# Optimization experiments

Hardware: AMD Instinct MI355X
Metric: run time of the kernel (lower is better)

## Reference

```python
import jax, jax.numpy as jnp
import numpy as np

E, H, BLOCK = 1024, 64, 2048

def setup_inputs() -> dict:
    key = jax.random.key(0)
    kx, kk, kq, kv = jax.random.split(key, 4)
    s = 1.0 / np.sqrt(E)
    return {
        "x": jax.random.normal(kx, (16, 2048, E), dtype=jnp.float32),
        "Wk": jax.random.uniform(kk, (E, H), jnp.float32, -s, s),
        "Wq": jax.random.uniform(kq, (E, H), jnp.float32, -s, s),
        "Wv": jax.random.uniform(kv, (E, H), jnp.float32, -s, s),
    }

def reference(x, Wk, Wq, Wv):
    B, T, C = x.shape
    k = x @ Wk  # [B,T,H]
    q = x @ Wq
    v = x @ Wv
    scale = jnp.asarray(H, x.dtype) ** -0.5
    wei = jnp.einsum("bth,bsh->bts", q, k) * scale  # [B,T,T]
    causal = jnp.tril(jnp.ones((T, T), dtype=bool))
    wei = jnp.where(causal, wei, -jnp.inf)
    wei = jax.nn.softmax(wei, axis=-1)
    # dropout is identity in eval mode
    return jnp.einsum("bts,bsh->bth", wei, v)
```

## Files before the change

### kernel.cpp

```cpp
#include <hip/hip_runtime.h>


typedef __bf16 bf16x8 __attribute__((ext_vector_type(8)));
typedef __bf16 bf16x4 __attribute__((ext_vector_type(4)));
typedef float f32x4 __attribute__((ext_vector_type(4)));

constexpr int kE = 1024;
constexpr int kH = 64;
constexpr int kT = 2048;
constexpr int kB = 16;
constexpr int kM = kB * kT;
constexpr float kQScale = 0.125f * 1.44269504088896340736f;

#define MFMA16(a, b, c) __builtin_amdgcn_mfma_f32_16x16x32_bf16((a), (b), (c), 0, 0, 0)

__global__ __launch_bounds__(256)
void prep_w(const float* __restrict__ Wq, const float* __restrict__ Wk,
            const float* __restrict__ Wv, __bf16* __restrict__ WbT)
{
    __shared__ float tl[64][65];
    const int mat = blockIdx.x >> 4;
    const int k0 = (blockIdx.x & 15) * 64;
    const float* src = (mat == 0) ? Wq : (mat == 1) ? Wk : Wv;

    const int t = threadIdx.x;
    const int kr = t >> 2;
    const int cg = (t & 3) * 16;
    #pragma unroll
    for (int i = 0; i < 4; ++i) {
        float4 v = *(const float4*)&src[(size_t)(k0 + kr) * kH + cg + 4 * i];
        tl[cg + 4 * i + 0][kr] = v.x;
        tl[cg + 4 * i + 1][kr] = v.y;
        tl[cg + 4 * i + 2][kr] = v.z;
        tl[cg + 4 * i + 3][kr] = v.w;
    }
    __syncthreads();
    const int nl = t >> 2;
    const int kg = (t & 3) * 16;
    bf16x8 o0, o1;
    #pragma unroll
    for (int j = 0; j < 8; ++j) {
        o0[j] = (__bf16)tl[nl][kg + j];
        o1[j] = (__bf16)tl[nl][kg + 8 + j];
    }
    *(bf16x8*)&WbT[(size_t)(mat * 64 + nl) * kE + k0 + kg] = o0;
    *(bf16x8*)&WbT[(size_t)(mat * 64 + nl) * kE + k0 + kg + 8] = o1;
}

__global__ __launch_bounds__(256)
void qkv(const float* __restrict__ x, const __bf16* __restrict__ WbT,
         __bf16* __restrict__ qo, __bf16* __restrict__ ko, __bf16* __restrict__ vT)
{
    __shared__ __align__(16) __bf16 As[64][72];
    __shared__ __align__(16) __bf16 Bs[192][72];

    const int t = threadIdx.x;
    const int lane = t & 63;
    const int w = t >> 6;
    const int l15 = lane & 15;
    const int q = lane >> 4;
    const int row0 = blockIdx.x * 64;

    f32x4 acc[4][3];
    #pragma unroll
    for (int mt = 0; mt < 4; ++mt)
        #pragma unroll
        for (int nt = 0; nt < 3; ++nt) acc[mt][nt] = (f32x4){0.f, 0.f, 0.f, 0.f};

    const int sm = t >> 2;
    const int sc = (t & 3) * 16;

    for (int k0 = 0; k0 < kE; k0 += 64) {
        {
            float4 v0 = *(const float4*)&x[(size_t)(row0 + sm) * kE + k0 + sc];
            float4 v1 = *(const float4*)&x[(size_t)(row0 + sm) * kE + k0 + sc + 4];
            float4 v2 = *(const float4*)&x[(size_t)(row0 + sm) * kE + k0 + sc + 8];
            float4 v3 = *(const float4*)&x[(size_t)(row0 + sm) * kE + k0 + sc + 12];
            bf16x8 b0, b1;
            b0[0] = (__bf16)v0.x; b0[1] = (__bf16)v0.y; b0[2] = (__bf16)v0.z; b0[3] = (__bf16)v0.w;
            b0[4] = (__bf16)v1.x; b0[5] = (__bf16)v1.y; b0[6] = (__bf16)v1.z; b0[7] = (__bf16)v1.w;
            b1[0] = (__bf16)v2.x; b1[1] = (__bf16)v2.y; b1[2] = (__bf16)v2.z; b1[3] = (__bf16)v2.w;
            b1[4] = (__bf16)v3.x; b1[5] = (__bf16)v3.y; b1[6] = (__bf16)v3.z; b1[7] = (__bf16)v3.w;
            *(bf16x8*)&As[sm][sc] = b0;
            *(bf16x8*)&As[sm][sc + 8] = b1;
        }
        #pragma unroll
        for (int j = 0; j < 6; ++j) {
            int id = t + 256 * j;
            int n = id >> 3;
            int kc = (id & 7) * 8;
            *(bf16x8*)&Bs[n][kc] = *(const bf16x8*)&WbT[(size_t)n * kE + k0 + kc];
        }
        __syncthreads();

        #pragma unroll
        for (int ks = 0; ks < 2; ++ks) {
            bf16x8 a4[4];
            #pragma unroll
            for (int mt = 0; mt < 4; ++mt)
                a4[mt] = *(const bf16x8*)&As[mt * 16 + l15][ks * 32 + q * 8];
            #pragma unroll
            for (int nt = 0; nt < 3; ++nt) {
                bf16x8 b = *(const bf16x8*)&Bs[w * 48 + nt * 16 + l15][ks * 32 + q * 8];
                #pragma unroll
                for (int mt = 0; mt < 4; ++mt)
                    acc[mt][nt] = MFMA16(a4[mt], b, acc[mt][nt]);
            }
        }
        __syncthreads();
    }

    const int batch = row0 >> 11;
    const int tr0 = row0 & 2047;
    #pragma unroll
    for (int nt = 0; nt < 3; ++nt) {
        const int col0 = w * 48 + nt * 16;
        const int mat = col0 >> 6;
        const int c = (col0 & 63) + l15;
        if (mat == 2) {
            #pragma unroll
            for (int mt = 0; mt < 4; ++mt) {
                const int trow = tr0 + mt * 16 + q * 4;
                bf16x4 pk;
                #pragma unroll
                for (int r = 0; r < 4; ++r) pk[r] = (__bf16)acc[mt][nt][r];
                *(bf16x4*)&vT[((size_t)batch * kH + c) * kT + trow] = pk;
            }
        } else {
            __bf16* dst = (mat == 0) ? qo : ko;
            const float sc_ = (mat == 0) ? kQScale : 1.0f;
            #pragma unroll
            for (int mt = 0; mt < 4; ++mt)
                #pragma unroll
                for (int r = 0; r < 4; ++r) {
                    const size_t row = row0 + mt * 16 + q * 4 + r;
                    dst[row * kH + c] = (__bf16)(acc[mt][nt][r] * sc_);
                }
        }
    }
}

__device__ __forceinline__ void load_kfrag(bf16x8 kf[8], const __bf16* kb,
                                           int s0, int l15, int Q)
{
    #pragma unroll
    for (int ks = 0; ks < 2; ++ks)
        #pragma unroll
        for (int nt = 0; nt < 4; ++nt)
            kf[ks * 4 + nt] =
                *(const bf16x8*)&kb[(size_t)(s0 + nt * 16 + l15) * kH + ks * 32 + Q * 8];
}

__global__ __launch_bounds__(64)
void attn(const __bf16* __restrict__ qm, const __bf16* __restrict__ km,
          const __bf16* __restrict__ vT, float* __restrict__ out)
{
    __shared__ __align__(16) __bf16 Ps[16][72];

    const int lane = threadIdx.x;
    const int l15 = lane & 15;
    const int Q = lane >> 4;

    const int batch = blockIdx.x & 15;
    const int q16 = 127 - (blockIdx.x >> 4);
    const int qrow = q16 * 16 + l15;
    const int last = q16 >> 2;

    const __bf16* qb = qm + (size_t)batch * kT * kH;
    const __bf16* kb = km + (size_t)batch * kT * kH;
    const __bf16* vb = vT + (size_t)batch * kH * kT;

    bf16x8 aq[2];
    aq[0] = *(const bf16x8*)&qb[(size_t)qrow * kH + Q * 8];
    aq[1] = *(const bf16x8*)&qb[(size_t)qrow * kH + 32 + Q * 8];

    f32x4 O[4];
    #pragma unroll
    for (int i = 0; i < 4; ++i) O[i] = (f32x4){0.f, 0.f, 0.f, 0.f};
    float m_ = -3.0e38f, l_ = 0.f;

    bf16x8 kfa[8], kfb[8];
    load_kfrag(kfa, kb, 0, l15, Q);

    auto step = [&](bf16x8 (&kcur)[8], bf16x8 (&knxt)[8], int kt) {
        const int s0 = kt * 64;
        bf16x8 vf[8];
        #pragma unroll
        for (int ht = 0; ht < 4; ++ht)
            #pragma unroll
            for (int ss = 0; ss < 2; ++ss)
                vf[ht * 2 + ss] =
                    *(const bf16x8*)&vb[(size_t)(ht * 16 + l15) * kT + s0 + ss * 32 + Q * 8];
        if (kt < last) load_kfrag(knxt, kb, s0 + 64, l15, Q);

        f32x4 sacc[4];
        #pragma unroll
        for (int nt = 0; nt < 4; ++nt) sacc[nt] = (f32x4){0.f, 0.f, 0.f, 0.f};
        #pragma unroll
        for (int ks = 0; ks < 2; ++ks)
            #pragma unroll
            for (int nt = 0; nt < 4; ++nt)
                sacc[nt] = MFMA16(kcur[ks * 4 + nt], aq[ks], sacc[nt]);

        if (kt == last) {
            #pragma unroll
            for (int nt = 0; nt < 4; ++nt)
                #pragma unroll
                for (int r = 0; r < 4; ++r)
                    if (s0 + nt * 16 + Q * 4 + r > qrow) sacc[nt][r] = -3.0e38f;
        }

        float mx = sacc[0][0];
        #pragma unroll
        for (int nt = 0; nt < 4; ++nt)
            #pragma unroll
            for (int r = 0; r < 4; ++r) mx = fmaxf(mx, sacc[nt][r]);
        mx = fmaxf(mx, __shfl_xor(mx, 16));
        mx = fmaxf(mx, __shfl_xor(mx, 32));
        const float mnew = fmaxf(m_, mx);
        const float alpha = __builtin_amdgcn_exp2f(m_ - mnew);
        float rs = 0.f;
        #pragma unroll
        for (int nt = 0; nt < 4; ++nt)
            #pragma unroll
            for (int r = 0; r < 4; ++r) {
                const float p = __builtin_amdgcn_exp2f(sacc[nt][r] - mnew);
                sacc[nt][r] = p;
                rs += p;
            }
        rs += __shfl_xor(rs, 16);
        rs += __shfl_xor(rs, 32);
        l_ = l_ * alpha + rs;
        m_ = mnew;
        #pragma unroll
        for (int ht = 0; ht < 4; ++ht) O[ht] *= alpha;

        #pragma unroll
        for (int nt = 0; nt < 4; ++nt) {
            bf16x4 pk;
            #pragma unroll
            for (int r = 0; r < 4; ++r) pk[r] = (__bf16)sacc[nt][r];
            *(bf16x4*)&Ps[l15][nt * 16 + Q * 4] = pk;
        }
        bf16x8 pb0 = *(const bf16x8*)&Ps[l15][Q * 8];
        bf16x8 pb1 = *(const bf16x8*)&Ps[l15][32 + Q * 8];

        #pragma unroll
        for (int ht = 0; ht < 4; ++ht) {
            O[ht] = MFMA16(vf[ht * 2 + 0], pb0, O[ht]);
            O[ht] = MFMA16(vf[ht * 2 + 1], pb1, O[ht]);
        }
    };

    for (int kt = 0; kt <= last; kt += 2) {
        step(kfa, kfb, kt);
        if (kt + 1 <= last) step(kfb, kfa, kt + 1);
    }

    const float inv = 1.0f / l_;
    float* orow = out + ((size_t)batch * kT + qrow) * kH;
    #pragma unroll
    for (int ht = 0; ht < 4; ++ht) {
        float4 o4;
        o4.x = O[ht][0] * inv; o4.y = O[ht][1] * inv;
        o4.z = O[ht][2] * inv; o4.w = O[ht][3] * inv;
        *(float4*)&orow[ht * 16 + Q * 4] = o4;
    }
}

extern "C" void kernel_launch(void* const* d_in, const int* in_sizes, int n_in,
                              void* d_out, int out_size, void* d_ws, size_t ws_size,
                              hipStream_t stream)
{
    (void)in_sizes; (void)n_in; (void)out_size; (void)ws_size;
    const float* x  = (const float*)d_in[0];
    const float* Wk = (const float*)d_in[1];
    const float* Wq = (const float*)d_in[2];
    const float* Wv = (const float*)d_in[3];

    __bf16* WbT = (__bf16*)d_ws;
    __bf16* qb  = WbT + (size_t)192 * kE;
    __bf16* kbuf = qb + (size_t)kM * kH;
    __bf16* vT   = kbuf + (size_t)kM * kH;

    prep_w<<<48, 256, 0, stream>>>(Wq, Wk, Wv, WbT);
    qkv<<<kM / 64, 256, 0, stream>>>(x, WbT, qb, kbuf, vT);
    attn<<<kB * 128, 64, 0, stream>>>(qb, kbuf, vT, (float*)d_out);
}
```

Before: 272.2 us.

## Split attention over KV chunks with a reduction pass and prefetch QKV GEMM tiles

The attention kernel now splits each 16-row query block's KV range into chunks of up to 8 tiles, each handled by its own workgroup. Partial O, m and l values go to workspace and a new reduction kernel rescales and combines them. This targets poor load balance and the long serial KV loop of the causal kernel, at the cost of extra global traffic, one more launch and losing the K register double-buffering. The QKV projection also halves its row tile to 32 for more workgroups and prefetches the next x/W tile into registers during compute.

```diff
diff --git a/kernel.cpp b/kernel.cpp
--- a/kernel.cpp
+++ b/kernel.cpp
@@ -51,7 +51,7 @@
 void qkv(const float* __restrict__ x, const __bf16* __restrict__ WbT,
          __bf16* __restrict__ qo, __bf16* __restrict__ ko, __bf16* __restrict__ vT)
 {
-    __shared__ __align__(16) __bf16 As[64][72];
+    __shared__ __align__(16) __bf16 As[32][72];
     __shared__ __align__(16) __bf16 Bs[192][72];
 
     const int t = threadIdx.x;
@@ -59,51 +59,64 @@
     const int w = t >> 6;
     const int l15 = lane & 15;
     const int q = lane >> 4;
-    const int row0 = blockIdx.x * 64;
-
-    f32x4 acc[4][3];
-    #pragma unroll
-    for (int mt = 0; mt < 4; ++mt)
+    const int row0 = blockIdx.x * 32;
+
+    f32x4 acc[2][3];
+    #pragma unroll
+    for (int mt = 0; mt < 2; ++mt)
         #pragma unroll
         for (int nt = 0; nt < 3; ++nt) acc[mt][nt] = (f32x4){0.f, 0.f, 0.f, 0.f};
 
-    const int sm = t >> 2;
-    const int sc = (t & 3) * 16;
-
-    for (int k0 = 0; k0 < kE; k0 += 64) {
-        {
-            float4 v0 = *(const float4*)&x[(size_t)(row0 + sm) * kE + k0 + sc];
-            float4 v1 = *(const float4*)&x[(size_t)(row0 + sm) * kE + k0 + sc + 4];
-            float4 v2 = *(const float4*)&x[(size_t)(row0 + sm) * kE + k0 + sc + 8];
-            float4 v3 = *(const float4*)&x[(size_t)(row0 + sm) * kE + k0 + sc + 12];
-            bf16x8 b0, b1;
-            b0[0] = (__bf16)v0.x; b0[1] = (__bf16)v0.y; b0[2] = (__bf16)v0.z; b0[3] = (__bf16)v0.w;
-            b0[4] = (__bf16)v1.x; b0[5] = (__bf16)v1.y; b0[6] = (__bf16)v1.z; b0[7] = (__bf16)v1.w;
-            b1[0] = (__bf16)v2.x; b1[1] = (__bf16)v2.y; b1[2] = (__bf16)v2.z; b1[3] = (__bf16)v2.w;
-            b1[4] = (__bf16)v3.x; b1[5] = (__bf16)v3.y; b1[6] = (__bf16)v3.z; b1[7] = (__bf16)v3.w;
-            *(bf16x8*)&As[sm][sc] = b0;
-            *(bf16x8*)&As[sm][sc + 8] = b1;
-        }
+    const int ar = t >> 3;
+    const int ac = (t & 7) * 8;
+
+    float4 a0, a1;
+    bf16x8 breg[6];
+    {
+        const float* ap = &x[(size_t)(row0 + ar) * kE + ac];
+        a0 = *(const float4*)ap;
+        a1 = *(const float4*)(ap + 4);
         #pragma unroll
         for (int j = 0; j < 6; ++j) {
             int id = t + 256 * j;
-            int n = id >> 3;
-            int kc = (id & 7) * 8;
-            *(bf16x8*)&Bs[n][kc] = *(const bf16x8*)&WbT[(size_t)n * kE + k0 + kc];
+            breg[j] = *(const bf16x8*)&WbT[(size_t)(id >> 3) * kE + (id & 7) * 8];
+        }
+    }
+
+    for (int k0 = 0; k0 < kE; k0 += 64) {
+        bf16x8 ab;
+        ab[0] = (__bf16)a0.x; ab[1] = (__bf16)a0.y; ab[2] = (__bf16)a0.z; ab[3] = (__bf16)a0.w;
+        ab[4] = (__bf16)a1.x; ab[5] = (__bf16)a1.y; ab[6] = (__bf16)a1.z; ab[7] = (__bf16)a1.w;
+        *(bf16x8*)&As[ar][ac] = ab;
+        #pragma unroll
+        for (int j = 0; j < 6; ++j) {
+            int id = t + 256 * j;
+            *(bf16x8*)&Bs[id >> 3][(id & 7) * 8] = breg[j];
         }
         __syncthreads();
 
+        if (k0 + 64 < kE) {
+            const float* ap = &x[(size_t)(row0 + ar) * kE + k0 + 64 + ac];
+            a0 = *(const float4*)ap;
+            a1 = *(const float4*)(ap + 4);
+            #pragma unroll
+            for (int j = 0; j < 6; ++j) {
+                int id = t + 256 * j;
+                breg[j] = *(const bf16x8*)&WbT[(size_t)(id >> 3) * kE + k0 + 64 + (id & 7) * 8];
+            }
+        }
+
         #pragma unroll
         for (int ks = 0; ks < 2; ++ks) {
-            bf16x8 a4[4];
-            #pragma unroll
-            for (int mt = 0; mt < 4; ++mt)
+            bf16x8 a4[2];
+            #pragma unroll
+            for (int mt = 0; mt < 2; ++mt)
                 a4[mt] = *(const bf16x8*)&As[mt * 16 + l15][ks * 32 + q * 8];
             #pragma unroll
             for (int nt = 0; nt < 3; ++nt) {
                 bf16x8 b = *(const bf16x8*)&Bs[w * 48 + nt * 16 + l15][ks * 32 + q * 8];
                 #pragma unroll
-                for (int mt = 0; mt < 4; ++mt)
+                for (int mt = 0; mt < 2; ++mt)
                     acc[mt][nt] = MFMA16(a4[mt], b, acc[mt][nt]);
             }
         }
@@ -119,7 +132,7 @@
         const int c = (col0 & 63) + l15;
         if (mat == 2) {
             #pragma unroll
-            for (int mt = 0; mt < 4; ++mt) {
+            for (int mt = 0; mt < 2; ++mt) {
                 const int trow = tr0 + mt * 16 + q * 4;
                 bf16x4 pk;
                 #pragma unroll
@@ -130,7 +143,7 @@
             __bf16* dst = (mat == 0) ? qo : ko;
             const float sc_ = (mat == 0) ? kQScale : 1.0f;
             #pragma unroll
-            for (int mt = 0; mt < 4; ++mt)
+            for (int mt = 0; mt < 2; ++mt)
                 #pragma unroll
                 for (int r = 0; r < 4; ++r) {
                     const size_t row = row0 + mt * 16 + q * 4 + r;
@@ -140,20 +153,10 @@
     }
 }
 
-__device__ __forceinline__ void load_kfrag(bf16x8 kf[8], const __bf16* kb,
-                                           int s0, int l15, int Q)
-{
-    #pragma unroll
-    for (int ks = 0; ks < 2; ++ks)
-        #pragma unroll
-        for (int nt = 0; nt < 4; ++nt)
-            kf[ks * 4 + nt] =
-                *(const bf16x8*)&kb[(size_t)(s0 + nt * 16 + l15) * kH + ks * 32 + Q * 8];
-}
-
-__global__ __launch_bounds__(64)
-void attn(const __bf16* __restrict__ qm, const __bf16* __restrict__ km,
-          const __bf16* __restrict__ vT, float* __restrict__ out)
+__global__ __launch_bounds__(64, 4)
+void attn_part(const __bf16* __restrict__ qm, const __bf16* __restrict__ km,
+               const __bf16* __restrict__ vT, float* __restrict__ pO,
+               float* __restrict__ pml)
 {
     __shared__ __align__(16) __bf16 Ps[16][72];
 
@@ -161,10 +164,16 @@
     const int l15 = lane & 15;
     const int Q = lane >> 4;
 
-    const int batch = blockIdx.x & 15;
-    const int q16 = 127 - (blockIdx.x >> 4);
+    const int bid = blockIdx.x;
+    const int c = bid & 3;
+    const int q16 = 127 - ((bid >> 2) & 127);
+    const int batch = bid >> 9;
+    const int last = q16 >> 2;
+    const int nch = (last + 8) >> 3;
+    if (c >= nch) return;
+    const int kt0 = c * 8;
+    const int kt1 = min(kt0 + 8, last + 1);
     const int qrow = q16 * 16 + l15;
-    const int last = q16 >> 2;
 
     const __bf16* qb = qm + (size_t)batch * kT * kH;
     const __bf16* kb = km + (size_t)batch * kT * kH;
@@ -179,19 +188,21 @@
     for (int i = 0; i < 4; ++i) O[i] = (f32x4){0.f, 0.f, 0.f, 0.f};
     float m_ = -3.0e38f, l_ = 0.f;
 
-    bf16x8 kfa[8], kfb[8];
-    load_kfrag(kfa, kb, 0, l15, Q);
-
-    auto step = [&](bf16x8 (&kcur)[8], bf16x8 (&knxt)[8], int kt) {
+    for (int kt = kt0; kt < kt1; ++kt) {
         const int s0 = kt * 64;
-        bf16x8 vf[8];
+        bf16x8 kf[8], vf[8];
+        #pragma unroll
+        for (int ks = 0; ks < 2; ++ks)
+            #pragma unroll
+            for (int nt = 0; nt < 4; ++nt)
+                kf[ks * 4 + nt] =
+                    *(const bf16x8*)&kb[(size_t)(s0 + nt * 16 + l15) * kH + ks * 32 + Q * 8];
         #pragma unroll
         for (int ht = 0; ht < 4; ++ht)
             #pragma unroll
             for (int ss = 0; ss < 2; ++ss)
                 vf[ht * 2 + ss] =
                     *(const bf16x8*)&vb[(size_t)(ht * 16 + l15) * kT + s0 + ss * 32 + Q * 8];
-        if (kt < last) load_kfrag(knxt, kb, s0 + 64, l15, Q);
 
         f32x4 sacc[4];
         #pragma unroll
@@ -200,7 +211,7 @@
         for (int ks = 0; ks < 2; ++ks)
             #pragma unroll
             for (int nt = 0; nt < 4; ++nt)
-                sacc[nt] = MFMA16(kcur[ks * 4 + nt], aq[ks], sacc[nt]);
+                sacc[nt] = MFMA16(kf[ks * 4 + nt], aq[ks], sacc[nt]);
 
         if (kt == last) {
             #pragma unroll
@@ -250,15 +261,59 @@
             O[ht] = MFMA16(vf[ht * 2 + 0], pb0, O[ht]);
             O[ht] = MFMA16(vf[ht * 2 + 1], pb1, O[ht]);
         }
-    };
-
-    for (int kt = 0; kt <= last; kt += 2) {
-        step(kfa, kfb, kt);
-        if (kt + 1 <= last) step(kfb, kfa, kt + 1);
-    }
-
-    const float inv = 1.0f / l_;
-    float* orow = out + ((size_t)batch * kT + qrow) * kH;
+    }
+
+    const int task = (batch * 128 + q16) * 4 + c;
+    float* po = pO + ((size_t)task * 64 + lane) * 16;
+    #pragma unroll
+    for (int ht = 0; ht < 4; ++ht) {
+        float4 o4;
+        o4.x = O[ht][0]; o4.y = O[ht][1]; o4.z = O[ht][2]; o4.w = O[ht][3];
+        *(float4*)&po[ht * 4] = o4;
+    }
+    if (Q == 0) {
+        pml[task * 32 + l15 * 2] = m_;
+        pml[task * 32 + l15 * 2 + 1] = l_;
+    }
+}
+
+__global__ __launch_bounds__(64)
+void attn_red(const float* __restrict__ pO, const float* __restrict__ pml,
+              float* __restrict__ out)
+{
+    const int lane = threadIdx.x;
+    const int l15 = lane & 15;
+    const int Q = lane >> 4;
+    const int q16 = blockIdx.x & 127;
+    const int batch = blockIdx.x >> 7;
+    const int nch = ((q16 >> 2) + 8) >> 3;
+    const int base = (batch * 128 + q16) * 4;
+
+    float M = -3.0e38f;
+    for (int c = 0; c < nch; ++c)
+        M = fmaxf(M, pml[(base + c) * 32 + l15 * 2]);
+
+    float L = 0.f;
+    f32x4 O[4];
+    #pragma unroll
+    for (int i = 0; i < 4; ++i) O[i] = (f32x4){0.f, 0.f, 0.f, 0.f};
+
+    for (int c = 0; c < nch; ++c) {
+        const float mc = pml[(base + c) * 32 + l15 * 2];
+        const float lc = pml[(base + c) * 32 + l15 * 2 + 1];
+        const float sc = __builtin_amdgcn_exp2f(mc - M);
+        L += sc * lc;
+        const float* po = pO + ((size_t)(base + c) * 64 + lane) * 16;
+        #pragma unroll
+        for (int ht = 0; ht < 4; ++ht) {
+            float4 o4 = *(const float4*)&po[ht * 4];
+            O[ht][0] += sc * o4.x; O[ht][1] += sc * o4.y;
+            O[ht][2] += sc * o4.z; O[ht][3] += sc * o4.w;
+        }
+    }
+
+    const float inv = 1.0f / L;
+    float* orow = out + ((size_t)batch * kT + q16 * 16 + l15) * kH;
     #pragma unroll
     for (int ht = 0; ht < 4; ++ht) {
         float4 o4;
@@ -279,11 +334,14 @@
     const float* Wv = (const float*)d_in[3];
 
     __bf16* WbT = (__bf16*)d_ws;
-    __bf16* qb  = WbT + (size_t)192 * kE;
+    __bf16* qb   = WbT + (size_t)192 * kE;
     __bf16* kbuf = qb + (size_t)kM * kH;
     __bf16* vT   = kbuf + (size_t)kM * kH;
+    float*  pO   = (float*)(vT + (size_t)kM * kH);
+    float*  pml  = pO + (size_t)8192 * 64 * 16;
 
     prep_w<<<48, 256, 0, stream>>>(Wq, Wk, Wv, WbT);
-    qkv<<<kM / 64, 256, 0, stream>>>(x, WbT, qb, kbuf, vT);
-    attn<<<kB * 128, 64, 0, stream>>>(qb, kbuf, vT, (float*)d_out);
-}
+    qkv<<<kM / 32, 256, 0, stream>>>(x, WbT, qb, kbuf, vT);
+    attn_part<<<16 * 128 * 4, 64, 0, stream>>>(qb, kbuf, vT, pO, pml);
+    attn_red<<<16 * 128, 64, 0, stream>>>(pO, pml, (float*)d_out);
+}
```

New measurement: 330.5 us. +21.4%, slower.

## Stage QKV and attention tiles via async global-to-LDS loads with swizzling

Applied to the files above, without the earlier changes.

The QKV GEMM now double-buffers x and weight tiles in LDS using direct global-to-LDS loads, with XOR swizzled layouts. It keeps x as fp32 in LDS and converts it to bf16 at fragment-read time. The attention kernel stages each K/V tile into swizzled LDS the same way, prefetching the next tile while computing, and changes block-to-(batch,query) mapping and launch bounds. The goal is to overlap global memory latency with MFMA work and cut register-held prefetch. In exchange the QKV stage needs twice the LDS and more conversion work per fragment read, and the attention loop drops the register double-buffering and inserts explicit waits.

```diff
diff --git a/kernel.cpp b/kernel.cpp
--- a/kernel.cpp
+++ b/kernel.cpp
@@ -13,6 +13,12 @@
 constexpr float kQScale = 0.125f * 1.44269504088896340736f;
 
 #define MFMA16(a, b, c) __builtin_amdgcn_mfma_f32_16x16x32_bf16((a), (b), (c), 0, 0, 0)
+
+__device__ __forceinline__ void gl_lds16(const void* g, void* l) {
+    __builtin_amdgcn_global_load_lds(
+        (const __attribute__((address_space(1))) void*)g,
+        (__attribute__((address_space(3))) void*)l, 16, 0, 0);
+}
 
 __global__ __launch_bounds__(256)
 void prep_w(const float* __restrict__ Wq, const float* __restrict__ Wk,
@@ -51,14 +57,14 @@
 void qkv(const float* __restrict__ x, const __bf16* __restrict__ WbT,
          __bf16* __restrict__ qo, __bf16* __restrict__ ko, __bf16* __restrict__ vT)
 {
-    __shared__ __align__(16) __bf16 As[64][72];
-    __shared__ __align__(16) __bf16 Bs[192][72];
+    __shared__ __align__(16) char Ab[2][16384];
+    __shared__ __align__(16) char Bb[2][24576];
 
     const int t = threadIdx.x;
     const int lane = t & 63;
     const int w = t >> 6;
     const int l15 = lane & 15;
-    const int q = lane >> 4;
+    const int Q = lane >> 4;
     const int row0 = blockIdx.x * 64;
 
     f32x4 acc[4][3];
@@ -67,41 +73,49 @@
         #pragma unroll
         for (int nt = 0; nt < 3; ++nt) acc[mt][nt] = (f32x4){0.f, 0.f, 0.f, 0.f};
 
-    const int sm = t >> 2;
-    const int sc = (t & 3) * 16;
-
-    for (int k0 = 0; k0 < kE; k0 += 64) {
-        {
-            float4 v0 = *(const float4*)&x[(size_t)(row0 + sm) * kE + k0 + sc];
-            float4 v1 = *(const float4*)&x[(size_t)(row0 + sm) * kE + k0 + sc + 4];
-            float4 v2 = *(const float4*)&x[(size_t)(row0 + sm) * kE + k0 + sc + 8];
-            float4 v3 = *(const float4*)&x[(size_t)(row0 + sm) * kE + k0 + sc + 12];
-            bf16x8 b0, b1;
-            b0[0] = (__bf16)v0.x; b0[1] = (__bf16)v0.y; b0[2] = (__bf16)v0.z; b0[3] = (__bf16)v0.w;
-            b0[4] = (__bf16)v1.x; b0[5] = (__bf16)v1.y; b0[6] = (__bf16)v1.z; b0[7] = (__bf16)v1.w;
-            b1[0] = (__bf16)v2.x; b1[1] = (__bf16)v2.y; b1[2] = (__bf16)v2.z; b1[3] = (__bf16)v2.w;
-            b1[4] = (__bf16)v3.x; b1[5] = (__bf16)v3.y; b1[6] = (__bf16)v3.z; b1[7] = (__bf16)v3.w;
-            *(bf16x8*)&As[sm][sc] = b0;
-            *(bf16x8*)&As[sm][sc + 8] = b1;
-        }
-        #pragma unroll
-        for (int j = 0; j < 6; ++j) {
-            int id = t + 256 * j;
-            int n = id >> 3;
-            int kc = (id & 7) * 8;
-            *(bf16x8*)&Bs[n][kc] = *(const bf16x8*)&WbT[(size_t)n * kE + k0 + kc];
-        }
-        __syncthreads();
+    auto stage = [&](int p, int k0) {
+        #pragma unroll
+        for (int i = 0; i < 4; ++i) {
+            const int row = (w * 4 + i) * 4 + (lane >> 4);
+            const int g = (lane & 15) ^ (i * 4 + (lane >> 4));
+            gl_lds16(&x[(size_t)(row0 + row) * kE + k0 + g * 4],
+                     &Ab[p][(w * 4 + i) * 1024]);
+        }
+        #pragma unroll
+        for (int i = 0; i < 6; ++i) {
+            const int n = (w * 6 + i) * 8 + (lane >> 3);
+            const int g = (lane & 7) ^ (lane >> 3);
+            gl_lds16(&WbT[(size_t)n * kE + k0 + g * 8],
+                     &Bb[p][(w * 6 + i) * 1024]);
+        }
+    };
+
+    stage(0, 0);
+    __syncthreads();
+
+    for (int c = 0; c < 16; ++c) {
+        const int p = c & 1;
+        if (c < 15) stage(1 - p, (c + 1) * 64);
 
         #pragma unroll
         for (int ks = 0; ks < 2; ++ks) {
             bf16x8 a4[4];
             #pragma unroll
-            for (int mt = 0; mt < 4; ++mt)
-                a4[mt] = *(const bf16x8*)&As[mt * 16 + l15][ks * 32 + q * 8];
+            for (int mt = 0; mt < 4; ++mt) {
+                const int row = mt * 16 + l15;
+                float4 u0 = *(const float4*)&Ab[p][row * 256 + ((ks * 8 + Q * 2 + 0) ^ l15) * 16];
+                float4 u1 = *(const float4*)&Ab[p][row * 256 + ((ks * 8 + Q * 2 + 1) ^ l15) * 16];
+                bf16x8 a;
+                a[0] = (__bf16)u0.x; a[1] = (__bf16)u0.y;
+                a[2] = (__bf16)u0.z; a[3] = (__bf16)u0.w;
+                a[4] = (__bf16)u1.x; a[5] = (__bf16)u1.y;
+                a[6] = (__bf16)u1.z; a[7] = (__bf16)u1.w;
+                a4[mt] = a;
+            }
             #pragma unroll
             for (int nt = 0; nt < 3; ++nt) {
-                bf16x8 b = *(const bf16x8*)&Bs[w * 48 + nt * 16 + l15][ks * 32 + q * 8];
+                const int n = w * 48 + nt * 16 + l15;
+                bf16x8 b = *(const bf16x8*)&Bb[p][n * 128 + (((ks * 4 + Q) ^ (l15 & 7)) * 16)];
                 #pragma unroll
                 for (int mt = 0; mt < 4; ++mt)
                     acc[mt][nt] = MFMA16(a4[mt], b, acc[mt][nt]);
@@ -120,7 +134,7 @@
         if (mat == 2) {
             #pragma unroll
             for (int mt = 0; mt < 4; ++mt) {
-                const int trow = tr0 + mt * 16 + q * 4;
+                const int trow = tr0 + mt * 16 + Q * 4;
                 bf16x4 pk;
                 #pragma unroll
                 for (int r = 0; r < 4; ++r) pk[r] = (__bf16)acc[mt][nt][r];
@@ -133,36 +147,27 @@
             for (int mt = 0; mt < 4; ++mt)
                 #pragma unroll
                 for (int r = 0; r < 4; ++r) {
-                    const size_t row = row0 + mt * 16 + q * 4 + r;
+                    const size_t row = row0 + mt * 16 + Q * 4 + r;
                     dst[row * kH + c] = (__bf16)(acc[mt][nt][r] * sc_);
                 }
         }
     }
 }
 
-__device__ __forceinline__ void load_kfrag(bf16x8 kf[8], const __bf16* kb,
-                                           int s0, int l15, int Q)
-{
-    #pragma unroll
-    for (int ks = 0; ks < 2; ++ks)
-        #pragma unroll
-        for (int nt = 0; nt < 4; ++nt)
-            kf[ks * 4 + nt] =
-                *(const bf16x8*)&kb[(size_t)(s0 + nt * 16 + l15) * kH + ks * 32 + Q * 8];
-}
-
-__global__ __launch_bounds__(64)
+__global__ __launch_bounds__(64, 2)
 void attn(const __bf16* __restrict__ qm, const __bf16* __restrict__ km,
           const __bf16* __restrict__ vT, float* __restrict__ out)
 {
+    __shared__ __align__(16) char Kb[8192];
+    __shared__ __align__(16) char Vb[8192];
     __shared__ __align__(16) __bf16 Ps[16][72];
 
     const int lane = threadIdx.x;
     const int l15 = lane & 15;
     const int Q = lane >> 4;
 
-    const int batch = blockIdx.x & 15;
-    const int q16 = 127 - (blockIdx.x >> 4);
+    const int batch = blockIdx.x >> 7;
+    const int q16 = 127 - (blockIdx.x & 127);
     const int qrow = q16 * 16 + l15;
     const int last = q16 >> 2;
 
@@ -170,6 +175,16 @@
     const __bf16* kb = km + (size_t)batch * kT * kH;
     const __bf16* vb = vT + (size_t)batch * kH * kT;
 
+    auto stage = [&](int s0) {
+        #pragma unroll
+        for (int i = 0; i < 8; ++i) {
+            const int n = i * 8 + (lane >> 3);
+            const int g = (lane & 7) ^ (lane >> 3);
+            gl_lds16(&kb[(size_t)(s0 + n) * kH + g * 8], &Kb[i * 1024]);
+            gl_lds16(&vb[(size_t)n * kT + s0 + g * 8], &Vb[i * 1024]);
+        }
+    };
+
     bf16x8 aq[2];
     aq[0] = *(const bf16x8*)&qb[(size_t)qrow * kH + Q * 8];
     aq[1] = *(const bf16x8*)&qb[(size_t)qrow * kH + 32 + Q * 8];
@@ -179,19 +194,26 @@
     for (int i = 0; i < 4; ++i) O[i] = (f32x4){0.f, 0.f, 0.f, 0.f};
     float m_ = -3.0e38f, l_ = 0.f;
 
-    bf16x8 kfa[8], kfb[8];
-    load_kfrag(kfa, kb, 0, l15, Q);
-
-    auto step = [&](bf16x8 (&kcur)[8], bf16x8 (&knxt)[8], int kt) {
-        const int s0 = kt * 64;
-        bf16x8 vf[8];
+    stage(0);
+    asm volatile("s_waitcnt vmcnt(0)" ::: "memory");
+
+    for (int kt = 0; kt <= last; ++kt) {
+        bf16x8 kf[8], vf[8];
+        #pragma unroll
+        for (int ks = 0; ks < 2; ++ks)
+            #pragma unroll
+            for (int nt = 0; nt < 4; ++nt)
+                kf[ks * 4 + nt] = *(const bf16x8*)
+                    &Kb[(nt * 16 + l15) * 128 + (((ks * 4 + Q) ^ (l15 & 7)) * 16)];
         #pragma unroll
         for (int ht = 0; ht < 4; ++ht)
             #pragma unroll
             for (int ss = 0; ss < 2; ++ss)
-                vf[ht * 2 + ss] =
-                    *(const bf16x8*)&vb[(size_t)(ht * 16 + l15) * kT + s0 + ss * 32 + Q * 8];
-        if (kt < last) load_kfrag(knxt, kb, s0 + 64, l15, Q);
+                vf[ht * 2 + ss] = *(const bf16x8*)
+                    &Vb[(ht * 16 + l15) * 128 + (((ss * 4 + Q) ^ (l15 & 7)) * 16)];
+        asm volatile("s_waitcnt lgkmcnt(0)" ::: "memory");
+
+        if (kt < last) stage((kt + 1) * 64);
 
         f32x4 sacc[4];
         #pragma unroll
@@ -200,9 +222,10 @@
         for (int ks = 0; ks < 2; ++ks)
             #pragma unroll
             for (int nt = 0; nt < 4; ++nt)
-                sacc[nt] = MFMA16(kcur[ks * 4 + nt], aq[ks], sacc[nt]);
+                sacc[nt] = MFMA16(kf[ks * 4 + nt], aq[ks], sacc[nt]);
 
         if (kt == last) {
+            const int s0 = kt * 64;
             #pragma unroll
             for (int nt = 0; nt < 4; ++nt)
                 #pragma unroll
@@ -224,9 +247,9 @@
         for (int nt = 0; nt < 4; ++nt)
             #pragma unroll
             for (int r = 0; r < 4; ++r) {
-                const float p = __builtin_amdgcn_exp2f(sacc[nt][r] - mnew);
-                sacc[nt][r] = p;
-                rs += p;
+                const float pv = __builtin_amdgcn_exp2f(sacc[nt][r] - mnew);
+                sacc[nt][r] = pv;
+                rs += pv;
             }
         rs += __shfl_xor(rs, 16);
         rs += __shfl_xor(rs, 32);
@@ -250,11 +273,8 @@
             O[ht] = MFMA16(vf[ht * 2 + 0], pb0, O[ht]);
             O[ht] = MFMA16(vf[ht * 2 + 1], pb1, O[ht]);
         }
-    };
-
-    for (int kt = 0; kt <= last; kt += 2) {
-        step(kfa, kfb, kt);
-        if (kt + 1 <= last) step(kfb, kfa, kt + 1);
+
+        asm volatile("s_waitcnt vmcnt(0)" ::: "memory");
     }
 
     const float inv = 1.0f / l_;
@@ -278,8 +298,8 @@
     const float* Wq = (const float*)d_in[2];
     const float* Wv = (const float*)d_in[3];
 
-    __bf16* WbT = (__bf16*)d_ws;
-    __bf16* qb  = WbT + (size_t)192 * kE;
+    __bf16* WbT  = (__bf16*)d_ws;
+    __bf16* qb   = WbT + (size_t)192 * kE;
     __bf16* kbuf = qb + (size_t)kM * kH;
     __bf16* vT   = kbuf + (size_t)kM * kH;
 
```

After: 259.2 us. 4.8% less time.
